# Kernel tuning notes

Measured on AMD Instinct MI355X. Metric: run time of the kernel, lower is better.

The kernel has to match this reference:

```python
import jax, jax.numpy as jnp
import numpy as np

DIM = 2048
N_HEADS = 16
N_KV_HEADS = 4
ROPE_BASE = 10000.0
QK_GAIN_INIT = 1.0
B, T = 4, 2048


def setup_inputs() -> dict:
    key = jax.random.key(0)
    ks = jax.random.split(key, 5)
    head_dim = DIM // N_HEADS
    kv_dim = N_KV_HEADS * head_dim
    x = jax.random.normal(ks[0], (B, T, DIM), dtype=jnp.float32)
    wq = jax.random.normal(ks[1], (DIM, DIM), dtype=jnp.float32) * 0.02
    wk = jax.random.normal(ks[2], (kv_dim, DIM), dtype=jnp.float32) * 0.02
    wv = jax.random.normal(ks[3], (kv_dim, DIM), dtype=jnp.float32) * 0.02
    wo = jax.random.normal(ks[4], (DIM, DIM), dtype=jnp.float32) * 0.02
    q_gain = jnp.full((N_HEADS,), QK_GAIN_INIT, dtype=jnp.float32)
    k_gain = jnp.full((N_KV_HEADS,), QK_GAIN_INIT, dtype=jnp.float32)
    return {"x": x, "wq": wq, "wk": wk, "wv": wv, "wo": wo,
            "q_gain": q_gain, "k_gain": k_gain}


def _rope_tables(T, head_dim, dtype):
    # inv_freq over even indices, freqs = outer(t, inv_freq) -> [T, head_dim//2]
    inv_freq = ROPE_BASE ** (-jnp.arange(0, head_dim, 2, dtype=jnp.float32) / head_dim)
    freqs = jnp.arange(T, dtype=jnp.float32)[:, None] * inv_freq[None, :]
    return jnp.cos(freqs).astype(dtype), jnp.sin(freqs).astype(dtype)


def _apply_rotary(x, cos, sin):
    # x: [..., T, head_dim]; cos/sin: [T, head_dim//2] broadcast over leading dims
    half = x.shape[-1] // 2
    x1, x2 = x[..., :half], x[..., half:]
    return jnp.concatenate((x1 * cos + x2 * sin, -x1 * sin + x2 * cos), axis=-1)


def reference(x, wq, wk, wv, wo, q_gain, k_gain):
    Bx, Tx, C = x.shape
    H, KV = N_HEADS, N_KV_HEADS
    D = C // H
    G = H // KV  # query groups per kv head

    q = (x @ wq.T).reshape(Bx, Tx, H, D)    # [B,T,H,D]
    k = (x @ wk.T).reshape(Bx, Tx, KV, D)   # [B,T,KV,D]
    v = (x @ wv.T).reshape(Bx, Tx, KV, D)

    q = q * q_gain[None, None, :, None]
    k = k * k_gain[None, None, :, None]

    cos, sin = _rope_tables(Tx, D, x.dtype)
    q = _apply_rotary(q.transpose(0, 2, 1, 3), cos, sin)  # [B,H,T,D]
    k = _apply_rotary(k.transpose(0, 2, 1, 3), cos, sin)  # [B,KV,T,D]
    v = v.transpose(0, 2, 1, 3)                            # [B,KV,T,D]

    # GQA without materializing repeated k/v: group query heads per kv head
    q = q.reshape(Bx, KV, G, Tx, D)
    scale = 1.0 / jnp.sqrt(jnp.array(D, dtype=x.dtype))
    scores = jnp.einsum('bkgtd,bksd->bkgts', q, k) * scale  # [B,KV,G,T,T]
    causal = jnp.tril(jnp.ones((Tx, Tx), dtype=bool))
    scores = jnp.where(causal, scores, jnp.finfo(scores.dtype).min)
    attn = jax.nn.softmax(scores, axis=-1)
    y = jnp.einsum('bkgts,bksd->bkgtd', attn, v)            # [B,KV,G,T,D]
    y = y.reshape(Bx, H, Tx, D).transpose(0, 2, 1, 3).reshape(Bx, Tx, C)
    return y @ wo.T
```

## Files before the change

kernel.cpp:

```cpp
#include <hip/hip_runtime.h>
#include <hip/hip_bf16.h>

typedef __bf16 bf16x8 __attribute__((ext_vector_type(8)));
typedef float f32x4 __attribute__((ext_vector_type(4)));

#define DIMC 2048
#define HD   128
#define NH   16
#define NKV  4
#define BSZ  4
#define TSZ  2048
#define MROWS (BSZ * TSZ)
#define NQKV  (DIMC + 2 * NKV * HD)


__device__ __forceinline__ void async_copy16(const void* g, void* l) {
  __builtin_amdgcn_global_load_lds(
      (const __attribute__((address_space(1))) void*)g,
      (__attribute__((address_space(3))) void*)l, 16, 0, 0);
}


__global__ void cvt_all(const float* __restrict__ x, const float* __restrict__ wq,
                        const float* __restrict__ wk, const float* __restrict__ wv,
                        const float* __restrict__ wo, __hip_bfloat16* __restrict__ dst) {
  const long n0 = (long)MROWS * DIMC;
  const long n1 = n0 + (long)DIMC * DIMC;
  const long n2 = n1 + (long)NKV * HD * DIMC;
  const long n3 = n2 + (long)NKV * HD * DIMC;
  long i = ((long)blockIdx.x * blockDim.x + threadIdx.x) * 4;
  const float* src; long off;
  if (i < n0)      { src = x;  off = i; }
  else if (i < n1) { src = wq; off = i - n0; }
  else if (i < n2) { src = wk; off = i - n1; }
  else if (i < n3) { src = wv; off = i - n2; }
  else             { src = wo; off = i - n3; }
  float4 v = *(const float4*)(src + off);
  union { __hip_bfloat16 b[4]; short4 s; } u;
  u.b[0] = __float2bfloat16(v.x);
  u.b[1] = __float2bfloat16(v.y);
  u.b[2] = __float2bfloat16(v.z);
  u.b[3] = __float2bfloat16(v.w);
  *(short4*)(dst + i) = u.s;
}


__global__ void rope_tab(float* __restrict__ ct, float* __restrict__ st) {
  int idx = blockIdx.x * blockDim.x + threadIdx.x;
  int d = idx & 63, t = idx >> 6;
  float inv = powf(10000.0f, -(float)d * (1.0f / 64.0f));
  float f = (float)t * inv;
  ct[idx] = cosf(f);
  st[idx] = sinf(f);
}


template <int OUT_BF16>
__global__ __launch_bounds__(256) void gemm_bt(
    const __hip_bfloat16* __restrict__ A, const __hip_bfloat16* __restrict__ Bw,
    void* __restrict__ Cv, int M, int N, int K) {
  __shared__ __align__(16) __hip_bfloat16 lsA[2][128 * 32];
  __shared__ __align__(16) __hip_bfloat16 lsB[2][128 * 32];
  const int tid = threadIdx.x;
  const int wave = tid >> 6, lane = tid & 63;
  const int quad = lane >> 4, l15 = lane & 15;
  const int m0 = blockIdx.y * 128, n0 = blockIdx.x * 128;
  const int wm = (wave >> 1) * 64, wn = (wave & 1) * 64;
  const int srow = lane >> 2;
  const int sgc = ((lane & 3) ^ (srow & 3)) * 8;
  const int fsw = (quad ^ (l15 & 3)) * 8;

  auto stage = [&](int k0, int buf) {
#pragma unroll
    for (int i = 0; i < 2; i++) {
      const int off = (wave * 2 + i) * 512;
      const int row = (wave * 2 + i) * 16 + srow;
      async_copy16(A + (long)(m0 + row) * K + k0 + sgc, &lsA[buf][off]);
      async_copy16(Bw + (long)(n0 + row) * K + k0 + sgc, &lsB[buf][off]);
    }
  };

  f32x4 acc[4][4] = {};
  const int nk = K >> 5;
  stage(0, 0);
  for (int kt = 0; kt < nk; kt++) {
    __syncthreads();
    if (kt + 1 < nk) stage((kt + 1) << 5, (kt + 1) & 1);
    const __hip_bfloat16* pA = lsA[kt & 1];
    const __hip_bfloat16* pB = lsB[kt & 1];
    bf16x8 af[4], bfr[4];
#pragma unroll
    for (int mi = 0; mi < 4; mi++)
      af[mi] = *(const bf16x8*)&pA[(wm + mi * 16 + l15) * 32 + fsw];
#pragma unroll
    for (int ni = 0; ni < 4; ni++)
      bfr[ni] = *(const bf16x8*)&pB[(wn + ni * 16 + l15) * 32 + fsw];
#pragma unroll
    for (int mi = 0; mi < 4; mi++)
#pragma unroll
      for (int ni = 0; ni < 4; ni++)
        acc[mi][ni] = __builtin_amdgcn_mfma_f32_16x16x32_bf16(af[mi], bfr[ni], acc[mi][ni], 0, 0, 0);
  }
#pragma unroll
  for (int mi = 0; mi < 4; mi++) {
#pragma unroll
    for (int r = 0; r < 4; r++) {
      const long row = m0 + wm + mi * 16 + quad * 4 + r;
      if (OUT_BF16) {
        __hip_bfloat16* Cb = (__hip_bfloat16*)Cv;
#pragma unroll
        for (int ni = 0; ni < 4; ni++)
          Cb[row * N + n0 + wn + ni * 16 + l15] = __float2bfloat16(acc[mi][ni][r]);
      } else {
        float* Cf = (float*)Cv;
#pragma unroll
        for (int ni = 0; ni < 4; ni++)
          Cf[row * N + n0 + wn + ni * 16 + l15] = acc[mi][ni][r];
      }
    }
  }
}


__global__ void rope_apply(const __hip_bfloat16* __restrict__ qkv,
                           const float* __restrict__ ct, const float* __restrict__ st,
                           const float* __restrict__ qg, const float* __restrict__ kg,
                           __hip_bfloat16* __restrict__ qr, __hip_bfloat16* __restrict__ kr) {
  const long QN = (long)BSZ * TSZ * NH * 64;
  long idx = (long)blockIdx.x * blockDim.x + threadIdx.x;
  if (idx < QN) {
    int d = idx & 63;
    int h = (int)((idx >> 6) & 15);
    long bt = idx >> 10;
    int t = (int)(bt & (TSZ - 1));
    long base = bt * NQKV + h * HD + d;
    float x1 = __bfloat162float(qkv[base]);
    float x2 = __bfloat162float(qkv[base + 64]);
    float c = ct[t * 64 + d], s = st[t * 64 + d];
    float g = qg[h] * 0.08838834764831845f * 1.4426950408889634f;
    long ob = ((bt >> 11) * NH + h) * ((long)TSZ * HD) + (long)t * HD + d;
    qr[ob]      = __float2bfloat16((x1 * c + x2 * s) * g);
    qr[ob + 64] = __float2bfloat16((-x1 * s + x2 * c) * g);
  } else {
    long j = idx - QN;
    int d = (int)(j & 63);
    int kv = (int)((j >> 6) & 3);
    long bt = j >> 8;
    int t = (int)(bt & (TSZ - 1));
    long base = bt * NQKV + DIMC + kv * HD + d;
    float x1 = __bfloat162float(qkv[base]);
    float x2 = __bfloat162float(qkv[base + 64]);
    float c = ct[t * 64 + d], s = st[t * 64 + d];
    float g = kg[kv];
    long ob = ((bt >> 11) * NKV + kv) * ((long)TSZ * HD) + (long)t * HD + d;
    kr[ob]      = __float2bfloat16((x1 * c + x2 * s) * g);
    kr[ob + 64] = __float2bfloat16((-x1 * s + x2 * c) * g);
  }
}


__global__ void vtrans(const __hip_bfloat16* __restrict__ qkv, __hip_bfloat16* __restrict__ vt) {
  __shared__ __hip_bfloat16 tile[64][65];
  const int bkv = blockIdx.z;
  const int b = bkv >> 2, kv = bkv & 3;
  const int t0 = blockIdx.y * 64, d0 = blockIdx.x * 64;
  const int tx = threadIdx.x, ty = threadIdx.y;
#pragma unroll
  for (int i = 0; i < 8; i++) {
    int t = ty + i * 8;
    tile[t][tx] = qkv[(long)(b * TSZ + t0 + t) * NQKV + DIMC + NKV * HD + kv * HD + d0 + tx];
  }
  __syncthreads();
#pragma unroll
  for (int i = 0; i < 8; i++) {
    int d = ty + i * 8;
    vt[((long)((b * NKV + kv) * HD + d0 + d)) * TSZ + t0 + tx] = tile[tx][d];
  }
}


__global__ __launch_bounds__(256, 2) void attn(
    const __hip_bfloat16* __restrict__ Q, const __hip_bfloat16* __restrict__ Kr,
    const __hip_bfloat16* __restrict__ Vt, __hip_bfloat16* __restrict__ Y) {
  __shared__ __align__(16) __hip_bfloat16 lds_v[2][64 * 128];
  __shared__ __align__(16) __hip_bfloat16 lds_k[64 * 128];
  __shared__ __align__(16) __hip_bfloat16 lds_p[4][32 * 64];
  const int qpair = blockIdx.x, bh = blockIdx.y;
  const int b = bh >> 4, h = bh & 15, kv = h >> 2;
  const int tid = threadIdx.x, wave = tid >> 6, lane = tid & 63;
  const int quad = lane >> 4, l15 = lane & 15, l7 = lane & 7;
  const __hip_bfloat16* Kp = Kr + (long)(b * NKV + kv) * TSZ * HD;
  const __hip_bfloat16* Vp = Vt + (long)(b * NKV + kv) * HD * TSZ;

  union { short u[8]; bf16x8 v; } ones;
#pragma unroll
  for (int i = 0; i < 8; i++) ones.u[i] = 0x3F80;

  auto stageK = [&](int j) {
#pragma unroll
    for (int i = 0; i < 4; i++) {
      int p = (i * 4 + wave) * 64 + lane;
      int row = p >> 4;
      int gc = (p & 15) ^ (row & 7);
      async_copy16(Kp + (long)j * 8192 + row * 128 + gc * 8, &lds_k[(i * 4 + wave) * 512]);
    }
  };
  auto stageV = [&](int j, int buf) {
#pragma unroll
    for (int i = 0; i < 4; i++) {
      int p = (i * 4 + wave) * 64 + lane;
      int d = p >> 3;
      int gc = (p & 7) ^ (d & 7);
      async_copy16(Vp + (long)d * TSZ + j * 64 + gc * 8, &lds_v[buf][(i * 4 + wave) * 512]);
    }
  };

  for (int half = 0; half < 2; half++) {
    const int qi = half ? (15 - qpair) : qpair;
    const __hip_bfloat16* Qp = Q + ((long)(b * NH + h) * TSZ + qi * 128 + wave * 32) * HD;
    bf16x8 aq[2][4];
#pragma unroll
    for (int ni = 0; ni < 2; ni++)
#pragma unroll
      for (int kk = 0; kk < 4; kk++)
        aq[ni][kk] = *(const bf16x8*)&Qp[(ni * 16 + l15) * HD + kk * 32 + quad * 8];

    f32x4 o[2][8] = {};
    f32x4 osum[2] = {};
    const int njt = 2 * qi + 2;

    stageV(0, 0);
    stageK(0);
    for (int j = 0; j < njt; j++) {
      __syncthreads();
      if (j + 1 < njt) stageV(j + 1, (j + 1) & 1);

      f32x4 s[4][2] = {};
#pragma unroll
      for (int kk = 0; kk < 4; kk++) {
        bf16x8 bk[4];
#pragma unroll
        for (int mi = 0; mi < 4; mi++)
          bk[mi] = *(const bf16x8*)&lds_k[(mi * 16 + l15) * 128 + ((kk * 4 + quad) ^ l7) * 8];
#pragma unroll
        for (int mi = 0; mi < 4; mi++)
#pragma unroll
          for (int ni = 0; ni < 2; ni++)
            s[mi][ni] = __builtin_amdgcn_mfma_f32_16x16x32_bf16(bk[mi], aq[ni][kk], s[mi][ni], 0, 0, 0);
      }

      const bool diag = (j >= 2 * qi);
#pragma unroll
      for (int mi = 0; mi < 4; mi++) {
#pragma unroll
        for (int ni = 0; ni < 2; ni++) {
          f32x4 p4;
          if (diag) {
            int qrow = qi * 128 + wave * 32 + ni * 16 + l15;
            int kbase = j * 64 + mi * 16 + quad * 4;
#pragma unroll
            for (int r = 0; r < 4; r++)
              p4[r] = (kbase + r <= qrow) ? exp2f(s[mi][ni][r]) : 0.f;
          } else {
#pragma unroll
            for (int r = 0; r < 4; r++) p4[r] = exp2f(s[mi][ni][r]);
          }
          const int c = mi * 4 + quad;
          const int addr = (ni * 16 + l15) * 64 + (((c >> 1) ^ l7) * 2 + (c & 1)) * 4;
          union { __hip_bfloat162 h2[2]; uint2 u; } pk;
          pk.h2[0] = __float22bfloat162_rn(float2{p4[0], p4[1]});
          pk.h2[1] = __float22bfloat162_rn(float2{p4[2], p4[3]});
          *(uint2*)&lds_p[wave][addr] = pk.u;
        }
      }

      asm volatile("s_barrier" ::: "memory");
      if (j + 1 < njt) stageK(j + 1);
      asm volatile("s_waitcnt lgkmcnt(0)" ::: "memory");

      const __hip_bfloat16* lv = lds_v[j & 1];
#pragma unroll
      for (int kk = 0; kk < 2; kk++) {
        bf16x8 ap[2];
#pragma unroll
        for (int mi = 0; mi < 2; mi++)
          ap[mi] = *(const bf16x8*)&lds_p[wave][(mi * 16 + l15) * 64 + ((kk * 4 + quad) ^ l7) * 8];
#pragma unroll
        for (int mi = 0; mi < 2; mi++)
          osum[mi] = __builtin_amdgcn_mfma_f32_16x16x32_bf16(ap[mi], ones.v, osum[mi], 0, 0, 0);
#pragma unroll
        for (int nd = 0; nd < 8; nd++) {
          bf16x8 bv = *(const bf16x8*)&lv[(nd * 16 + l15) * 64 + ((kk * 4 + quad) ^ l7) * 8];
#pragma unroll
          for (int mi = 0; mi < 2; mi++)
            o[mi][nd] = __builtin_amdgcn_mfma_f32_16x16x32_bf16(ap[mi], bv, o[mi][nd], 0, 0, 0);
        }
      }
    }

    const long yb0 = (long)b * TSZ + qi * 128 + wave * 32;
#pragma unroll
    for (int mi = 0; mi < 2; mi++) {
#pragma unroll
      for (int r = 0; r < 4; r++) {
        float inv = 1.0f / osum[mi][r];
        long row = yb0 + mi * 16 + quad * 4 + r;
#pragma unroll
        for (int nd = 0; nd < 8; nd++)
          Y[row * DIMC + h * HD + nd * 16 + l15] = __float2bfloat16(o[mi][nd][r] * inv);
      }
    }
    __syncthreads();
  }
}


extern "C" void kernel_launch(void* const* d_in, const int* in_sizes, int n_in,
                              void* d_out, int out_size, void* d_ws, size_t ws_size,
                              hipStream_t stream) {
  const float* x  = (const float*)d_in[0];
  const float* wq = (const float*)d_in[1];
  const float* wk = (const float*)d_in[2];
  const float* wv = (const float*)d_in[3];
  const float* wo = (const float*)d_in[4];
  const float* qg = (const float*)d_in[5];
  const float* kg = (const float*)d_in[6];

  char* ws = (char*)d_ws;
  size_t off = 0;
  auto alloc = [&](size_t bytes) {
    char* p = ws + off;
    off += (bytes + 255) & ~(size_t)255;
    return p;
  };
  __hip_bfloat16* xb    = (__hip_bfloat16*)alloc((size_t)MROWS * DIMC * 2);
  __hip_bfloat16* wqkvb = (__hip_bfloat16*)alloc((size_t)NQKV * DIMC * 2);
  __hip_bfloat16* wob   = (__hip_bfloat16*)alloc((size_t)DIMC * DIMC * 2);
  __hip_bfloat16* qkv   = (__hip_bfloat16*)alloc((size_t)MROWS * NQKV * 2);
  __hip_bfloat16* qr    = (__hip_bfloat16*)alloc((size_t)MROWS * DIMC * 2);
  __hip_bfloat16* kr    = (__hip_bfloat16*)alloc((size_t)BSZ * NKV * TSZ * HD * 2);
  __hip_bfloat16* vt    = (__hip_bfloat16*)alloc((size_t)BSZ * NKV * TSZ * HD * 2);
  float* ct = (float*)alloc((size_t)TSZ * 64 * 4);
  float* st = (float*)alloc((size_t)TSZ * 64 * 4);
  __hip_bfloat16* yb = xb;

  const long NCVT = (long)MROWS * DIMC + (long)DIMC * DIMC * 2 + (long)NKV * HD * DIMC * 2;
  cvt_all<<<NCVT / 1024, 256, 0, stream>>>(x, wq, wk, wv, wo, xb);
  rope_tab<<<TSZ * 64 / 256, 256, 0, stream>>>(ct, st);

  gemm_bt<1><<<dim3(NQKV / 128, MROWS / 128), 256, 0, stream>>>(xb, wqkvb, qkv, MROWS, NQKV, DIMC);

  const long QN = (long)BSZ * TSZ * NH * 64;
  const long KN = (long)BSZ * TSZ * NKV * 64;
  rope_apply<<<(QN + KN) / 256, 256, 0, stream>>>(qkv, ct, st, qg, kg, qr, kr);
  vtrans<<<dim3(HD / 64, TSZ / 64, BSZ * NKV), dim3(64, 8), 0, stream>>>(qkv, vt);

  attn<<<dim3(8, BSZ * NH), 256, 0, stream>>>(qr, kr, vt, yb);

  gemm_bt<0><<<dim3(DIMC / 128, MROWS / 128), 256, 0, stream>>>(yb, wob, d_out, MROWS, DIMC, DIMC);
}
```

Baseline: 473.0 us.

## Replace 128x128 GEMM with 256x256 eight-wave pipelined GEMM

Swaps the QKV and output-projection GEMMs to a 256x256 tile, 512-thread kernel with a K-step of 64. Global-to-LDS copies are split into quarter stages that are interleaved with the MFMA phases, using explicit waitcnt and barriers plus s_setprio around the MFMA blocks. It also adds XOR-swizzled LDS layout and a block-id remap for L2 locality. The aim is to raise arithmetic intensity and overlap loads with compute, at the cost of more registers, 128KB of LDS and a fragile hand-written sync schedule.

```diff
diff --git a/kernel.cpp b/kernel.cpp
--- a/kernel.cpp
+++ b/kernel.cpp
@@ -55,67 +55,143 @@
 }
 
 
+__device__ __forceinline__ void load_frags4(const __hip_bfloat16* p, int rbase,
+                                            int quad, int l7, int l15,
+                                            bf16x8 fr[4][2]) {
+#pragma unroll
+  for (int i = 0; i < 4; i++) {
+    const int r = rbase + i * 16 + l15;
+#pragma unroll
+    for (int kk = 0; kk < 2; kk++)
+      fr[i][kk] = *(const bf16x8*)&p[r * 64 + (((kk << 2) + quad) ^ l7) * 8];
+  }
+}
+
+__device__ __forceinline__ void mfma_quad(f32x4 acc[8][4], const bf16x8 a[4][2],
+                                          const bf16x8 b[4][2], int mb, int nb) {
+#pragma unroll
+  for (int kk = 0; kk < 2; kk++)
+#pragma unroll
+    for (int mi = 0; mi < 4; mi++)
+#pragma unroll
+      for (int ni = 0; ni < 2; ni++)
+        acc[mb + mi][nb + ni] = __builtin_amdgcn_mfma_f32_16x16x32_bf16(
+            a[mi][kk], b[nb + ni][kk], acc[mb + mi][nb + ni], 0, 0, 0);
+}
+
 template <int OUT_BF16>
-__global__ __launch_bounds__(256) void gemm_bt(
+__global__ __launch_bounds__(512, 2) void gemm256_bt(
     const __hip_bfloat16* __restrict__ A, const __hip_bfloat16* __restrict__ Bw,
     void* __restrict__ Cv, int M, int N, int K) {
-  __shared__ __align__(16) __hip_bfloat16 lsA[2][128 * 32];
-  __shared__ __align__(16) __hip_bfloat16 lsB[2][128 * 32];
+  __shared__ __align__(16) __hip_bfloat16 lsA[2][16384];
+  __shared__ __align__(16) __hip_bfloat16 lsB[2][16384];
   const int tid = threadIdx.x;
-  const int wave = tid >> 6, lane = tid & 63;
-  const int quad = lane >> 4, l15 = lane & 15;
-  const int m0 = blockIdx.y * 128, n0 = blockIdx.x * 128;
-  const int wm = (wave >> 1) * 64, wn = (wave & 1) * 64;
-  const int srow = lane >> 2;
-  const int sgc = ((lane & 3) ^ (srow & 3)) * 8;
-  const int fsw = (quad ^ (l15 & 3)) * 8;
-
-  auto stage = [&](int k0, int buf) {
-#pragma unroll
-    for (int i = 0; i < 2; i++) {
-      const int off = (wave * 2 + i) * 512;
-      const int row = (wave * 2 + i) * 16 + srow;
-      async_copy16(A + (long)(m0 + row) * K + k0 + sgc, &lsA[buf][off]);
-      async_copy16(Bw + (long)(n0 + row) * K + k0 + sgc, &lsB[buf][off]);
+  const int w = tid >> 6, lane = tid & 63;
+  const int quad = lane >> 4, l15 = lane & 15, l7 = lane & 7;
+  const int wr = w >> 2, wc = w & 3;
+  const int wrow = wr * 128, wcol = wc * 64;
+  const int wbase = w * 512;
+
+  const int nwg = gridDim.x * gridDim.y;
+  const int bid = blockIdx.y * gridDim.x + blockIdx.x;
+  const int sw = (bid & 7) * (nwg >> 3) + (bid >> 3);
+  const int m0 = (sw / gridDim.x) * 256, n0 = (sw % gridDim.x) * 256;
+
+  const int NTt = K >> 6;
+
+  const __hip_bfloat16 *gA0, *gA1, *gB0, *gB1;
+  {
+    const int p0 = tid, p1 = 512 + tid;
+    const int r0 = p0 >> 3, c0 = ((p0 & 7) ^ (r0 & 7)) * 8;
+    const int r1 = p1 >> 3, c1 = ((p1 & 7) ^ (r1 & 7)) * 8;
+    gA0 = A + (long)(m0 + r0) * K + c0;
+    gA1 = A + (long)(m0 + r1) * K + c1;
+    gB0 = Bw + (long)(n0 + r0) * K + c0;
+    gB1 = Bw + (long)(n0 + r1) * K + c1;
+  }
+  const long hstep = (long)128 * K;
+
+  auto stage_half = [&](int st) {
+    if (st >= 4 * NTt) return;
+    const int t2 = st >> 2, hf = st & 3;
+    const long koff = (long)(t2 << 6);
+    if (hf < 2) {
+      __hip_bfloat16* L = &lsB[t2 & 1][hf * 8192 + wbase];
+      const long o = (long)hf * hstep + koff;
+      async_copy16(gB0 + o, L);
+      async_copy16(gB1 + o, L + 4096);
+    } else {
+      __hip_bfloat16* L = &lsA[t2 & 1][(hf - 2) * 8192 + wbase];
+      const long o = (long)(hf - 2) * hstep + koff;
+      async_copy16(gA0 + o, L);
+      async_copy16(gA1 + o, L + 4096);
     }
   };
 
-  f32x4 acc[4][4] = {};
-  const int nk = K >> 5;
-  stage(0, 0);
-  for (int kt = 0; kt < nk; kt++) {
-    __syncthreads();
-    if (kt + 1 < nk) stage((kt + 1) << 5, (kt + 1) & 1);
-    const __hip_bfloat16* pA = lsA[kt & 1];
-    const __hip_bfloat16* pB = lsB[kt & 1];
-    bf16x8 af[4], bfr[4];
-#pragma unroll
-    for (int mi = 0; mi < 4; mi++)
-      af[mi] = *(const bf16x8*)&pA[(wm + mi * 16 + l15) * 32 + fsw];
-#pragma unroll
-    for (int ni = 0; ni < 4; ni++)
-      bfr[ni] = *(const bf16x8*)&pB[(wn + ni * 16 + l15) * 32 + fsw];
-#pragma unroll
-    for (int mi = 0; mi < 4; mi++)
-#pragma unroll
-      for (int ni = 0; ni < 4; ni++)
-        acc[mi][ni] = __builtin_amdgcn_mfma_f32_16x16x32_bf16(af[mi], bfr[ni], acc[mi][ni], 0, 0, 0);
-  }
-#pragma unroll
-  for (int mi = 0; mi < 4; mi++) {
+  f32x4 acc[8][4] = {};
+  bf16x8 a[4][2], b[4][2];
+
+#pragma unroll
+  for (int st = 0; st < 7; st++) stage_half(st);
+  asm volatile("s_waitcnt vmcnt(6)" ::: "memory");
+  __builtin_amdgcn_s_barrier();
+
+  for (int t = 0; t < NTt; t++) {
+    const __hip_bfloat16* pA = lsA[t & 1];
+    const __hip_bfloat16* pB = lsB[t & 1];
+
+    load_frags4(pA, wrow, quad, l7, l15, a);
+    load_frags4(pB, wcol, quad, l7, l15, b);
+    stage_half(4 * t + 7);
+    asm volatile("s_waitcnt lgkmcnt(8)" ::: "memory");
+    __builtin_amdgcn_s_barrier();
+    asm volatile("s_waitcnt lgkmcnt(0)" ::: "memory");
+    __builtin_amdgcn_s_setprio(1);
+    mfma_quad(acc, a, b, 0, 0);
+    __builtin_amdgcn_s_setprio(0);
+    __builtin_amdgcn_s_barrier();
+
+    stage_half(4 * t + 8);
+    __builtin_amdgcn_s_barrier();
+    __builtin_amdgcn_s_setprio(1);
+    mfma_quad(acc, a, b, 0, 2);
+    __builtin_amdgcn_s_setprio(0);
+    __builtin_amdgcn_s_barrier();
+
+    load_frags4(pA, wrow + 64, quad, l7, l15, a);
+    stage_half(4 * t + 9);
+    __builtin_amdgcn_s_barrier();
+    asm volatile("s_waitcnt lgkmcnt(0)" ::: "memory");
+    __builtin_amdgcn_s_setprio(1);
+    mfma_quad(acc, a, b, 4, 0);
+    __builtin_amdgcn_s_setprio(0);
+    __builtin_amdgcn_s_barrier();
+
+    stage_half(4 * t + 10);
+    __builtin_amdgcn_s_barrier();
+    __builtin_amdgcn_s_setprio(1);
+    mfma_quad(acc, a, b, 4, 2);
+    __builtin_amdgcn_s_setprio(0);
+    if (t < NTt - 3) asm volatile("s_waitcnt vmcnt(6)" ::: "memory");
+    else             asm volatile("s_waitcnt vmcnt(0)" ::: "memory");
+    __builtin_amdgcn_s_barrier();
+  }
+
+#pragma unroll
+  for (int mi = 0; mi < 8; mi++) {
 #pragma unroll
     for (int r = 0; r < 4; r++) {
-      const long row = m0 + wm + mi * 16 + quad * 4 + r;
+      const long row = m0 + wrow + mi * 16 + quad * 4 + r;
       if (OUT_BF16) {
         __hip_bfloat16* Cb = (__hip_bfloat16*)Cv;
 #pragma unroll
         for (int ni = 0; ni < 4; ni++)
-          Cb[row * N + n0 + wn + ni * 16 + l15] = __float2bfloat16(acc[mi][ni][r]);
+          Cb[row * N + n0 + wcol + ni * 16 + l15] = __float2bfloat16(acc[mi][ni][r]);
       } else {
         float* Cf = (float*)Cv;
 #pragma unroll
         for (int ni = 0; ni < 4; ni++)
-          Cf[row * N + n0 + wn + ni * 16 + l15] = acc[mi][ni][r];
+          Cf[row * N + n0 + wcol + ni * 16 + l15] = acc[mi][ni][r];
       }
     }
   }
@@ -348,7 +424,7 @@
   cvt_all<<<NCVT / 1024, 256, 0, stream>>>(x, wq, wk, wv, wo, xb);
   rope_tab<<<TSZ * 64 / 256, 256, 0, stream>>>(ct, st);
 
-  gemm_bt<1><<<dim3(NQKV / 128, MROWS / 128), 256, 0, stream>>>(xb, wqkvb, qkv, MROWS, NQKV, DIMC);
+  gemm256_bt<1><<<dim3(NQKV / 256, MROWS / 256), 512, 0, stream>>>(xb, wqkvb, qkv, MROWS, NQKV, DIMC);
 
   const long QN = (long)BSZ * TSZ * NH * 64;
   const long KN = (long)BSZ * TSZ * NKV * 64;
@@ -357,5 +433,5 @@
 
   attn<<<dim3(8, BSZ * NH), 256, 0, stream>>>(qr, kr, vt, yb);
 
-  gemm_bt<0><<<dim3(DIMC / 128, MROWS / 128), 256, 0, stream>>>(yb, wob, d_out, MROWS, DIMC, DIMC);
-}
+  gemm256_bt<0><<<dim3(DIMC / 256, MROWS / 256), 512, 0, stream>>>(yb, wob, d_out, MROWS, DIMC, DIMC);
+}
```

After: 456.8 us. 1.04x faster.
